# Performance work log

Hardware: AMD Instinct MI355X
Metric: run time of the kernel (lower is better)

## Reference

```python
import jax, jax.numpy as jnp
import numpy as np

B, D, E = 4096, 64, 1
NU, NI = 50000, 10000
H, HD = 4, 16          # MultiheadAttention(node_dim=64, num_heads=4)
GAMMA, LAM = 1.0, 0.5


def setup_inputs() -> dict:
    key = jax.random.key(0)
    ks = jax.random.split(key, 16)
    s = 0.05
    return {
        "u": jnp.arange(B, dtype=jnp.int32),                         # unique user ids
        "v": jax.random.randint(ks[0], (B,), 0, NI),
        "t": jax.random.normal(ks[1], (B,), jnp.float32),
        "delta_t": jax.random.uniform(ks[2], (B,), jnp.float32),
        "edge_feat": jax.random.normal(ks[3], (B, E), jnp.float32),
        "returns": jax.random.normal(ks[4], (NI,), jnp.float32),
        "cov_matrix": jax.random.normal(ks[5], (NI, NI), jnp.float32),
        "user_emb_w": jax.random.normal(ks[6], (NU, D), jnp.float32) * s,
        "item_emb_w": jax.random.normal(ks[7], (NI, D), jnp.float32) * s,
        "mem": jnp.zeros((NU, D), jnp.float32),                      # TGN memory (init zeros)
        "gru_w_ih": jax.random.normal(ks[8], (3 * D, 2 * D + 1 + E), jnp.float32) * s,
        "gru_w_hh": jax.random.normal(ks[9], (3 * D, D), jnp.float32) * s,
        "gru_b_ih": jnp.zeros((3 * D,), jnp.float32),
        "gru_b_hh": jnp.zeros((3 * D,), jnp.float32),
        "in_proj_w": jax.random.normal(ks[10], (3 * D, D), jnp.float32) * s,
        "in_proj_b": jnp.zeros((3 * D,), jnp.float32),
        "out_proj_w": jax.random.normal(ks[11], (D, D), jnp.float32) * s,
        "out_proj_b": jnp.zeros((D,), jnp.float32),
    }


def reference(u, v, t, delta_t, edge_feat, returns, cov_matrix,
              user_emb_w, item_emb_w, mem,
              gru_w_ih, gru_w_hh, gru_b_ih, gru_b_hh,
              in_proj_w, in_proj_b, out_proj_w, out_proj_b):
    u_emb = user_emb_w[u]                                  # [B, D]
    v_emb = item_emb_w[v]                                  # [B, D]

    # --- TGN memory update: gather -> GRUCell -> (scatter). u is unique per batch,
    # so the original per-node Python loop == one batched GRUCell step.
    msg = jnp.concatenate([u_emb, v_emb, delta_t[:, None], edge_feat], axis=1)  # [B, 2D+1+E]
    h = mem[u]                                             # [B, D]
    gi = msg @ gru_w_ih.T + gru_b_ih                       # [B, 3D]
    gh = h @ gru_w_hh.T + gru_b_hh                         # [B, 3D]
    i_r, i_z, i_n = jnp.split(gi, 3, axis=1)
    h_r, h_z, h_n = jnp.split(gh, 3, axis=1)
    r = jax.nn.sigmoid(i_r + h_r)
    z = jax.nn.sigmoid(i_z + h_z)
    n = jnp.tanh(i_n + r * h_n)
    h_new = (1.0 - z) * n + z * h                          # updated memory rows [B, D]

    # --- GraphAttention over a 2-token sequence [src, neighbor+edge]
    x = jnp.stack([u_emb, v_emb + edge_feat], axis=1)      # [B, 2, D] (edge_feat [B,1] broadcasts)
    qkv = x @ in_proj_w.T + in_proj_b                      # [B, 2, 3D]
    q, k, vv = jnp.split(qkv, 3, axis=-1)
    to_heads = lambda a: a.reshape(B, 2, H, HD).transpose(0, 2, 1, 3)  # [B, H, 2, HD]
    q, k, vv = to_heads(q), to_heads(k), to_heads(vv)
    attn = jax.nn.softmax(jnp.einsum("bhqd,bhkd->bhqk", q, k) * 0.25, axis=-1)  # 1/sqrt(16)
    o = jnp.einsum("bhqk,bhkd->bhqd", attn, vv).transpose(0, 2, 1, 3).reshape(B, 2, D)
    o = o @ out_proj_w.T + out_proj_b
    z_u = o[:, 0]                                          # [B, D]

    # --- portfolio scatter + MV scoring (portfolio starts empty; items added = v)
    cov_vals = cov_matrix[:, v].mean(axis=1)               # [NI] big irregular gather
    mv = returns / GAMMA - 0.5 * cov_vals                  # [NI]
    pref = jax.random.uniform(jax.random.key(42), (NI,), jnp.float32)
    combined = LAM * mv + (1.0 - LAM) * pref               # [NI]

    candidates = jnp.ones((B, NI), bool).at[jnp.arange(B), v].set(False)
    scores = jnp.where(candidates, combined[None, :], -jnp.inf)  # [B, NI]
    _, topk = jax.lax.top_k(scores, 4)
    pos_items = topk[:, 0]
    neg_items = topk[:, 1:4]
    return z_u, h_new, pos_items, neg_items
```

## Files before the change

### kernel.cpp

```cpp
#include <hip/hip_runtime.h>
#include <math.h>

#define BB_ 4096
#define DD_ 64
#define NI_ 10000

#define GRU_BLOCKS  256
#define ATT_BLOCKS  512
#define MV_BLOCKS   2500
#define BIG_BLOCKS  (GRU_BLOCKS + ATT_BLOCKS + MV_BLOCKS)

#define LDSF 13312

#define S1_BLOCKS 40

typedef unsigned long long u64;
typedef float v4f __attribute__((ext_vector_type(4)));

__device__ inline unsigned rotl32(unsigned x, unsigned r){ return (x<<r)|(x>>(32u-r)); }

__device__ inline float jax_uniform_key42(int i){
  const unsigned k0 = 0u, k1 = 42u;
  const unsigned ks2 = 0x1BD11BDAu ^ k0 ^ k1;
  unsigned x0 = 0u, x1 = (unsigned)i;
  unsigned ks[3] = {k0, k1, ks2};
  x0 += ks[0]; x1 += ks[1];
  const unsigned R0[4] = {13u,15u,26u,6u};
  const unsigned R1[4] = {17u,29u,16u,24u};
  #pragma unroll
  for (int it = 0; it < 5; ++it){
    const unsigned* R = (it & 1) ? R1 : R0;
    #pragma unroll
    for (int j = 0; j < 4; ++j){ x0 += x1; x1 = rotl32(x1, R[j]); x1 ^= x0; }
    x0 += ks[(it+1)%3];
    x1 += ks[(it+2)%3] + (unsigned)(it+1);
  }
  unsigned bits = x0 ^ x1;
  unsigned f = (bits >> 9) | 0x3F800000u;
  return __uint_as_float(f) - 1.0f;
}

__global__ __launch_bounds__(1024) void hist_kernel(
    const int* __restrict__ v, float* __restrict__ w_out)
{
  __shared__ float wl[NI_];
  const int tid = threadIdx.x;
  for (int i = tid; i < NI_; i += 1024) wl[i] = 0.0f;
  __syncthreads();
  for (int i = tid; i < BB_; i += 1024) atomicAdd(&wl[v[i]], 1.0f);
  __syncthreads();
  for (int i = tid; i < NI_; i += 1024) w_out[i] = wl[i];
}

__device__ inline float dot4v(v4f a, v4f b){
  return a.x*b.x + a.y*b.y + a.z*b.z + a.w*b.w;
}

__global__ __launch_bounds__(256, 3) void big_kernel(
    const int* __restrict__ u, const int* __restrict__ v,
    const float* __restrict__ delta_t, const float* __restrict__ edge_feat,
    const float* __restrict__ w_in, const float* __restrict__ returns,
    const float* __restrict__ cov, float* __restrict__ combined,
    const float* __restrict__ user_emb, const float* __restrict__ item_emb,
    const float* __restrict__ mem,
    const float* __restrict__ w_ih, const float* __restrict__ w_hh,
    const float* __restrict__ b_ih, const float* __restrict__ b_hh,
    const float* __restrict__ in_w, const float* __restrict__ in_b,
    const float* __restrict__ out_w, const float* __restrict__ out_b,
    float* __restrict__ h_new_out, float* __restrict__ z_out)
{
  __shared__ __align__(16) float S[LDSF];
  const int tid  = threadIdx.x;
  const int lane = tid & 63, wid = tid >> 6;
  const int bid  = blockIdx.x;

  if (bid >= GRU_BLOCKS + ATT_BLOCKS) {
    {
      const float4* src = (const float4*)w_in;
      float4* dst = (float4*)S;
      for (int i = tid; i < NI_/4; i += 256) dst[i] = src[i];
    }
    __syncthreads();

    const int row = (bid - (GRU_BLOCKS + ATT_BLOCKS)) * 4 + wid;
    const v4f* w4 = (const v4f*)S;
    const v4f* r4 = (const v4f*)(cov + (size_t)row * NI_);

    float a0 = 0.0f, a1 = 0.0f, a2 = 0.0f, a3 = 0.0f;
    int k = lane;
    #pragma unroll 1
    for (int it = 0; it < 9; ++it, k += 256) {
      v4f c0 = __builtin_nontemporal_load(&r4[k]);
      v4f c1 = __builtin_nontemporal_load(&r4[k+64]);
      v4f c2 = __builtin_nontemporal_load(&r4[k+128]);
      v4f c3 = __builtin_nontemporal_load(&r4[k+192]);
      v4f w0 = w4[k], w1 = w4[k+64], w2 = w4[k+128], w3 = w4[k+192];
      a0 += dot4v(c0, w0);
      a1 += dot4v(c1, w1);
      a2 += dot4v(c2, w2);
      a3 += dot4v(c3, w3);
    }
    #pragma unroll 1
    for (int it = 0; it < 3; ++it, k += 64) {
      v4f c0 = __builtin_nontemporal_load(&r4[k]);
      a0 += dot4v(c0, w4[k]);
    }
    if (lane < 4) {
      v4f c0 = __builtin_nontemporal_load(&r4[2496 + lane]);
      a1 += dot4v(c0, w4[2496 + lane]);
    }
    float acc = (a0 + a1) + (a2 + a3);
    #pragma unroll
    for (int off = 32; off > 0; off >>= 1) acc += __shfl_xor(acc, off);

    if (lane == 0) {
      float cov_val = acc * (1.0f / (float)BB_);
      float mv = returns[row] - 0.5f * cov_val;
      float pref = jax_uniform_key42(row);
      combined[row] = 0.5f * mv + 0.5f * pref;
    }
  } else if (bid < GRU_BLOCKS) {
    float* T  = S;
    float* BI = S + 12738;
    float* BH = S + 12930;
    const int rowbase = bid * 16 + wid * 4;

    if (tid < 192) { BI[tid] = b_ih[tid]; BH[tid] = b_hh[tid]; }

    float u_d[4], v_d[4], h_d[4], dt[4], ef[4];
    int bb[4];
    #pragma unroll
    for (int rr = 0; rr < 4; ++rr) {
      int b = rowbase + rr; bb[rr] = b;
      int uu = u[b], vv = v[b];
      u_d[rr] = user_emb[uu*64 + lane];
      v_d[rr] = item_emb[vv*64 + lane];
      h_d[rr] = mem[uu*64 + lane];
      dt[rr]  = delta_t[b];
      ef[rr]  = edge_feat[b];
    }

    for (int idx = tid; idx < 64*192; idx += 256) {
      int o = idx >> 6, j = idx & 63;
      T[j*193 + o] = w_ih[o*130 + j];
    }
    __syncthreads();

    float biR = BI[lane], biZ = BI[64+lane], biN = BI[128+lane];
    float bhR = BH[lane], bhZ = BH[64+lane], bhN = BH[128+lane];
    float accR[4], accZ[4], accN[4], hN[4];
    #pragma unroll
    for (int rr = 0; rr < 4; ++rr) { accR[rr]=biR+bhR; accZ[rr]=biZ+bhZ; accN[rr]=biN; hN[rr]=bhN; }

    for (int j = 0; j < 64; ++j) {
      float wR = T[j*193 + lane], wZ = T[j*193 + 64 + lane], wN = T[j*193 + 128 + lane];
      #pragma unroll
      for (int rr = 0; rr < 4; ++rr) {
        float m = __shfl(u_d[rr], j);
        accR[rr] = fmaf(wR, m, accR[rr]); accZ[rr] = fmaf(wZ, m, accZ[rr]); accN[rr] = fmaf(wN, m, accN[rr]);
      }
    }
    __syncthreads();

    for (int idx = tid; idx < 64*192; idx += 256) {
      int o = idx >> 6, j = idx & 63;
      T[j*193 + o] = w_ih[o*130 + 64 + j];
    }
    __syncthreads();
    for (int j = 0; j < 64; ++j) {
      float wR = T[j*193 + lane], wZ = T[j*193 + 64 + lane], wN = T[j*193 + 128 + lane];
      #pragma unroll
      for (int rr = 0; rr < 4; ++rr) {
        float m = __shfl(v_d[rr], j);
        accR[rr] = fmaf(wR, m, accR[rr]); accZ[rr] = fmaf(wZ, m, accZ[rr]); accN[rr] = fmaf(wN, m, accN[rr]);
      }
    }
    __syncthreads();

    for (int idx = tid; idx < 384; idx += 256) {
      int o = idx >> 1, c = idx & 1;
      T[c*193 + o] = w_ih[o*130 + 128 + c];
    }
    for (int idx = tid; idx < 64*192; idx += 256) {
      int o = idx >> 6, jj = idx & 63;
      T[(2+jj)*193 + o] = w_hh[idx];
    }
    __syncthreads();
    {
      float wR = T[lane], wZ = T[64 + lane], wN = T[128 + lane];
      float eR = T[193 + lane], eZ = T[193 + 64 + lane], eN = T[193 + 128 + lane];
      #pragma unroll
      for (int rr = 0; rr < 4; ++rr) {
        accR[rr] = fmaf(wR, dt[rr], accR[rr]); accZ[rr] = fmaf(wZ, dt[rr], accZ[rr]); accN[rr] = fmaf(wN, dt[rr], accN[rr]);
        accR[rr] = fmaf(eR, ef[rr], accR[rr]); accZ[rr] = fmaf(eZ, ef[rr], accZ[rr]); accN[rr] = fmaf(eN, ef[rr], accN[rr]);
      }
    }
    for (int jj = 0; jj < 64; ++jj) {
      int base = (2+jj)*193;
      float wR = T[base + lane], wZ = T[base + 64 + lane], wN = T[base + 128 + lane];
      #pragma unroll
      for (int rr = 0; rr < 4; ++rr) {
        float m = __shfl(h_d[rr], jj);
        accR[rr] = fmaf(wR, m, accR[rr]); accZ[rr] = fmaf(wZ, m, accZ[rr]); hN[rr] = fmaf(wN, m, hN[rr]);
      }
    }

    #pragma unroll
    for (int rr = 0; rr < 4; ++rr) {
      float r = 1.0f / (1.0f + expf(-accR[rr]));
      float z = 1.0f / (1.0f + expf(-accZ[rr]));
      float n = tanhf(accN[rr] + r * hN[rr]);
      float hn = (1.0f - z) * n + z * h_d[rr];
      h_new_out[bb[rr]*64 + lane] = hn;
    }
  } else {
    float* C    = S;
    float* OT   = S + 4160;
    float* BIN  = S + 8320;
    float* BOUT = S + 8512;
    const int abid = bid - GRU_BLOCKS;
    const int rowbase = abid * 8 + wid * 2;

    for (int idx = tid; idx < 64*64; idx += 256) {
      int k = idx >> 6, j = idx & 63;
      OT[j*65 + k] = out_w[idx];
    }
    if (tid < 192) BIN[tid] = in_b[tid];
    if (tid < 64)  BOUT[tid] = out_b[tid];

    float u_d[2], x1_d[2];
    int bb[2];
    #pragma unroll
    for (int rr = 0; rr < 2; ++rr) {
      int b = rowbase + rr; bb[rr] = b;
      int uu = u[b], vv = v[b];
      float ef = edge_feat[b];
      u_d[rr]  = user_emb[uu*64 + lane];
      x1_d[rr] = item_emb[vv*64 + lane] + ef;
    }

    float q0[2], k0[2], k1[2], v0[2], v1[2];

    for (int idx = tid; idx < 4096; idx += 256) {
      int o = idx >> 6, j = idx & 63;
      C[j*65 + o] = in_w[o*64 + j];
    }
    __syncthreads();
    {
      float bq = BIN[lane];
      #pragma unroll
      for (int rr = 0; rr < 2; ++rr) q0[rr] = bq;
      for (int j = 0; j < 64; ++j) {
        float wq = C[j*65 + lane];
        #pragma unroll
        for (int rr = 0; rr < 2; ++rr) q0[rr] = fmaf(wq, __shfl(u_d[rr], j), q0[rr]);
      }
    }
    __syncthreads();

    for (int idx = tid; idx < 4096; idx += 256) {
      int o = idx >> 6, j = idx & 63;
      C[j*65 + o] = in_w[(64+o)*64 + j];
    }
    __syncthreads();
    {
      float bk = BIN[64+lane];
      #pragma unroll
      for (int rr = 0; rr < 2; ++rr) { k0[rr] = bk; k1[rr] = bk; }
      for (int j = 0; j < 64; ++j) {
        float wk = C[j*65 + lane];
        #pragma unroll
        for (int rr = 0; rr < 2; ++rr) {
          k0[rr] = fmaf(wk, __shfl(u_d[rr], j),  k0[rr]);
          k1[rr] = fmaf(wk, __shfl(x1_d[rr], j), k1[rr]);
        }
      }
    }
    __syncthreads();

    for (int idx = tid; idx < 4096; idx += 256) {
      int o = idx >> 6, j = idx & 63;
      C[j*65 + o] = in_w[(128+o)*64 + j];
    }
    __syncthreads();
    {
      float bv = BIN[128+lane];
      #pragma unroll
      for (int rr = 0; rr < 2; ++rr) { v0[rr] = bv; v1[rr] = bv; }
      for (int j = 0; j < 64; ++j) {
        float wv = C[j*65 + lane];
        #pragma unroll
        for (int rr = 0; rr < 2; ++rr) {
          v0[rr] = fmaf(wv, __shfl(u_d[rr], j),  v0[rr]);
          v1[rr] = fmaf(wv, __shfl(x1_d[rr], j), v1[rr]);
        }
      }
    }

    #pragma unroll
    for (int rr = 0; rr < 2; ++rr) {
      float p0 = q0[rr]*k0[rr], p1 = q0[rr]*k1[rr];
      #pragma unroll
      for (int off = 1; off < 16; off <<= 1) { p0 += __shfl_xor(p0, off); p1 += __shfl_xor(p1, off); }
      float s0 = p0 * 0.25f, s1 = p1 * 0.25f;
      float m  = fmaxf(s0, s1);
      float e0 = expf(s0 - m), e1 = expf(s1 - m);
      float inv = 1.0f / (e0 + e1);
      float o_d = (e0 * v0[rr] + e1 * v1[rr]) * inv;
      float zacc = BOUT[lane];
      for (int j = 0; j < 64; ++j)
        zacc = fmaf(OT[j*65 + lane], __shfl(o_d, j), zacc);
      z_out[bb[rr]*64 + lane] = zacc;
    }
  }
}

__device__ inline u64 shfl_down_u64(u64 x, int off){
  unsigned lo = (unsigned)(x & 0xFFFFFFFFull), hi = (unsigned)(x >> 32);
  lo = __shfl_down(lo, off); hi = __shfl_down(hi, off);
  return ((u64)hi << 32) | (u64)lo;
}

__device__ inline u64 make_key(float val, int i){
  unsigned u = __float_as_uint(val);
  u ^= (u >> 31) ? 0xFFFFFFFFu : 0x80000000u;
  return ((u64)u << 32) | (u64)(0xFFFFFFFFu - (unsigned)i);
}

__global__ __launch_bounds__(256) void top5_stage1(
    const float* __restrict__ combined, u64* __restrict__ keys_out)
{
  __shared__ u64 redL[4];
  __shared__ u64 sel;
  const int tid = threadIdx.x, lane = tid & 63, wid = tid >> 6;
  const int i = blockIdx.x * 250 + tid;

  u64 key = 0ull;
  if (tid < 250 && i < NI_) key = make_key(combined[i], i);

  for (int r = 0; r < 5; ++r) {
    u64 best = key;
    #pragma unroll
    for (int off = 32; off > 0; off >>= 1) {
      u64 o = shfl_down_u64(best, off);
      if (o > best) best = o;
    }
    if (lane == 0) redL[wid] = best;
    __syncthreads();
    if (tid == 0) {
      u64 b = redL[0];
      for (int wv = 1; wv < 4; ++wv) if (redL[wv] > b) b = redL[wv];
      sel = b;
      keys_out[blockIdx.x * 5 + r] = b;
    }
    __syncthreads();
    if (key == sel) key = 0ull;
  }
}

__global__ __launch_bounds__(256) void top5_stage2(
    const u64* __restrict__ keys_in, const int* __restrict__ v,
    float* __restrict__ pos_out, float* __restrict__ neg_out)
{
  __shared__ u64 redL[4];
  __shared__ u64 sel;
  __shared__ int chosen[5];
  const int tid = threadIdx.x, lane = tid & 63, wid = tid >> 6;

  u64 key = (tid < 5 * S1_BLOCKS) ? keys_in[tid] : 0ull;

  for (int r = 0; r < 5; ++r) {
    u64 best = key;
    #pragma unroll
    for (int off = 32; off > 0; off >>= 1) {
      u64 o = shfl_down_u64(best, off);
      if (o > best) best = o;
    }
    if (lane == 0) redL[wid] = best;
    __syncthreads();
    if (tid == 0) {
      u64 b = redL[0];
      for (int wv = 1; wv < 4; ++wv) if (redL[wv] > b) b = redL[wv];
      sel = b;
      chosen[r] = (int)(0xFFFFFFFFu - (unsigned)(b & 0xFFFFFFFFull));
    }
    __syncthreads();
    if (key == sel) key = 0ull;
  }

  const int b = blockIdx.x * 256 + tid;
  int vb = v[b];
  int f[4]; int n = 0;
  #pragma unroll
  for (int c = 0; c < 5; ++c) { if (n < 4 && chosen[c] != vb) f[n++] = chosen[c]; }
  pos_out[b]       = (float)f[0];
  neg_out[b*3 + 0] = (float)f[1];
  neg_out[b*3 + 1] = (float)f[2];
  neg_out[b*3 + 2] = (float)f[3];
}

extern "C" void kernel_launch(void* const* d_in, const int* in_sizes, int n_in,
                              void* d_out, int out_size, void* d_ws, size_t ws_size,
                              hipStream_t stream)
{
  const int*   u        = (const int*)d_in[0];
  const int*   v        = (const int*)d_in[1];
  const float* delta_t  = (const float*)d_in[3];
  const float* edge_f   = (const float*)d_in[4];
  const float* returns  = (const float*)d_in[5];
  const float* cov      = (const float*)d_in[6];
  const float* user_emb = (const float*)d_in[7];
  const float* item_emb = (const float*)d_in[8];
  const float* mem      = (const float*)d_in[9];
  const float* w_ih     = (const float*)d_in[10];
  const float* w_hh     = (const float*)d_in[11];
  const float* b_ih     = (const float*)d_in[12];
  const float* b_hh     = (const float*)d_in[13];
  const float* in_w     = (const float*)d_in[14];
  const float* in_b     = (const float*)d_in[15];
  const float* out_w    = (const float*)d_in[16];
  const float* out_b    = (const float*)d_in[17];

  float* out     = (float*)d_out;
  float* z_out   = out;
  float* h_out   = out + BB_*DD_;
  float* pos_out = out + 2*BB_*DD_;
  float* neg_out = out + 2*BB_*DD_ + BB_;

  float* ws        = (float*)d_ws;
  float* w_hist    = ws;
  float* combined  = ws + 10240;
  u64*   keys      = (u64*)(ws + 20480);

  hipLaunchKernelGGL(hist_kernel, dim3(1), dim3(1024), 0, stream, v, w_hist);
  hipLaunchKernelGGL(big_kernel, dim3(BIG_BLOCKS), dim3(256), 0, stream,
                     u, v, delta_t, edge_f, w_hist, returns, cov, combined,
                     user_emb, item_emb, mem, w_ih, w_hh, b_ih, b_hh,
                     in_w, in_b, out_w, out_b, h_out, z_out);
  hipLaunchKernelGGL(top5_stage1, dim3(S1_BLOCKS), dim3(256), 0, stream,
                     combined, keys);
  hipLaunchKernelGGL(top5_stage2, dim3(16), dim3(256), 0, stream,
                     keys, v, pos_out, neg_out);
}
```

Measured before the change: 116.5 us.

## Shrink big_kernel LDS footprint to double occupancy

Cuts the shared-memory buffer roughly in half and raises the launch-bounds occupancy hint from 3 to 6 blocks per CU. The MV blocks now read the weight vector straight from global memory instead of staging it in LDS. The GRU blocks stream the combined weight columns through a 32-column LDS tile. The attention blocks reuse one LDS buffer for the output projection after the QKV pass. The intent is more concurrent waves to hide latency on the bandwidth-bound covariance stream, at the cost of extra barriers, extra global/L2 reads of the weights, and possible register pressure from the tighter bound.

```diff
diff --git a/kernel.cpp b/kernel.cpp
--- a/kernel.cpp
+++ b/kernel.cpp
@@ -10,7 +10,7 @@
 #define MV_BLOCKS   2500
 #define BIG_BLOCKS  (GRU_BLOCKS + ATT_BLOCKS + MV_BLOCKS)
 
-#define LDSF 13312
+#define LDSF 6560
 
 #define S1_BLOCKS 40
 
@@ -56,7 +56,7 @@
   return a.x*b.x + a.y*b.y + a.z*b.z + a.w*b.w;
 }
 
-__global__ __launch_bounds__(256, 3) void big_kernel(
+__global__ __launch_bounds__(256, 6) void big_kernel(
     const int* __restrict__ u, const int* __restrict__ v,
     const float* __restrict__ delta_t, const float* __restrict__ edge_feat,
     const float* __restrict__ w_in, const float* __restrict__ returns,
@@ -75,15 +75,8 @@
   const int bid  = blockIdx.x;
 
   if (bid >= GRU_BLOCKS + ATT_BLOCKS) {
-    {
-      const float4* src = (const float4*)w_in;
-      float4* dst = (float4*)S;
-      for (int i = tid; i < NI_/4; i += 256) dst[i] = src[i];
-    }
-    __syncthreads();
-
     const int row = (bid - (GRU_BLOCKS + ATT_BLOCKS)) * 4 + wid;
-    const v4f* w4 = (const v4f*)S;
+    const v4f* w4 = (const v4f*)w_in;
     const v4f* r4 = (const v4f*)(cov + (size_t)row * NI_);
 
     float a0 = 0.0f, a1 = 0.0f, a2 = 0.0f, a3 = 0.0f;
@@ -121,8 +114,8 @@
     }
   } else if (bid < GRU_BLOCKS) {
     float* T  = S;
-    float* BI = S + 12738;
-    float* BH = S + 12930;
+    float* BI = S + 6176;
+    float* BH = S + 6368;
     const int rowbase = bid * 16 + wid * 4;
 
     if (tid < 192) { BI[tid] = b_ih[tid]; BH[tid] = b_hh[tid]; }
@@ -140,68 +133,45 @@
       ef[rr]  = edge_feat[b];
     }
 
-    for (int idx = tid; idx < 64*192; idx += 256) {
-      int o = idx >> 6, j = idx & 63;
-      T[j*193 + o] = w_ih[o*130 + j];
-    }
-    __syncthreads();
-
-    float biR = BI[lane], biZ = BI[64+lane], biN = BI[128+lane];
-    float bhR = BH[lane], bhZ = BH[64+lane], bhN = BH[128+lane];
     float accR[4], accZ[4], accN[4], hN[4];
-    #pragma unroll
-    for (int rr = 0; rr < 4; ++rr) { accR[rr]=biR+bhR; accZ[rr]=biZ+bhZ; accN[rr]=biN; hN[rr]=bhN; }
-
-    for (int j = 0; j < 64; ++j) {
-      float wR = T[j*193 + lane], wZ = T[j*193 + 64 + lane], wN = T[j*193 + 128 + lane];
-      #pragma unroll
-      for (int rr = 0; rr < 4; ++rr) {
-        float m = __shfl(u_d[rr], j);
-        accR[rr] = fmaf(wR, m, accR[rr]); accZ[rr] = fmaf(wZ, m, accZ[rr]); accN[rr] = fmaf(wN, m, accN[rr]);
-      }
-    }
-    __syncthreads();
-
-    for (int idx = tid; idx < 64*192; idx += 256) {
-      int o = idx >> 6, j = idx & 63;
-      T[j*193 + o] = w_ih[o*130 + 64 + j];
-    }
-    __syncthreads();
-    for (int j = 0; j < 64; ++j) {
-      float wR = T[j*193 + lane], wZ = T[j*193 + 64 + lane], wN = T[j*193 + 128 + lane];
-      #pragma unroll
-      for (int rr = 0; rr < 4; ++rr) {
-        float m = __shfl(v_d[rr], j);
-        accR[rr] = fmaf(wR, m, accR[rr]); accZ[rr] = fmaf(wZ, m, accZ[rr]); accN[rr] = fmaf(wN, m, accN[rr]);
-      }
-    }
-    __syncthreads();
-
-    for (int idx = tid; idx < 384; idx += 256) {
-      int o = idx >> 1, c = idx & 1;
-      T[c*193 + o] = w_ih[o*130 + 128 + c];
-    }
-    for (int idx = tid; idx < 64*192; idx += 256) {
-      int o = idx >> 6, jj = idx & 63;
-      T[(2+jj)*193 + o] = w_hh[idx];
-    }
-    __syncthreads();
-    {
-      float wR = T[lane], wZ = T[64 + lane], wN = T[128 + lane];
-      float eR = T[193 + lane], eZ = T[193 + 64 + lane], eN = T[193 + 128 + lane];
-      #pragma unroll
-      for (int rr = 0; rr < 4; ++rr) {
-        accR[rr] = fmaf(wR, dt[rr], accR[rr]); accZ[rr] = fmaf(wZ, dt[rr], accZ[rr]); accN[rr] = fmaf(wN, dt[rr], accN[rr]);
-        accR[rr] = fmaf(eR, ef[rr], accR[rr]); accZ[rr] = fmaf(eZ, ef[rr], accZ[rr]); accN[rr] = fmaf(eN, ef[rr], accN[rr]);
-      }
-    }
-    for (int jj = 0; jj < 64; ++jj) {
-      int base = (2+jj)*193;
-      float wR = T[base + lane], wZ = T[base + 64 + lane], wN = T[base + 128 + lane];
-      #pragma unroll
-      for (int rr = 0; rr < 4; ++rr) {
-        float m = __shfl(h_d[rr], jj);
-        accR[rr] = fmaf(wR, m, accR[rr]); accZ[rr] = fmaf(wZ, m, accZ[rr]); hN[rr] = fmaf(wN, m, hN[rr]);
+    bool init = false;
+
+    for (int c = 0; c < 194; c += 32) {
+      const int ncols = (194 - c < 32) ? (194 - c) : 32;
+      __syncthreads();
+      for (int idx = tid; idx < ncols*192; idx += 256) {
+        int cc = idx / 192, o = idx - cc*192;
+        int col = c + cc;
+        T[cc*193 + o] = (col < 130) ? w_ih[o*130 + col] : w_hh[o*64 + (col-130)];
+      }
+      __syncthreads();
+
+      if (!init) {
+        init = true;
+        float biR = BI[lane], biZ = BI[64+lane], biN = BI[128+lane];
+        float bhR = BH[lane], bhZ = BH[64+lane], bhN = BH[128+lane];
+        #pragma unroll
+        for (int rr = 0; rr < 4; ++rr) { accR[rr]=biR+bhR; accZ[rr]=biZ+bhZ; accN[rr]=biN; hN[rr]=bhN; }
+      }
+
+      for (int cc = 0; cc < ncols; ++cc) {
+        const int col = c + cc;
+        float wR = T[cc*193 + lane], wZ = T[cc*193 + 64 + lane], wN = T[cc*193 + 128 + lane];
+        if (col < 130) {
+          #pragma unroll
+          for (int rr = 0; rr < 4; ++rr) {
+            float m = (col < 64)  ? __shfl(u_d[rr], col)
+                    : (col < 128) ? __shfl(v_d[rr], col-64)
+                    : (col == 128) ? dt[rr] : ef[rr];
+            accR[rr] = fmaf(wR, m, accR[rr]); accZ[rr] = fmaf(wZ, m, accZ[rr]); accN[rr] = fmaf(wN, m, accN[rr]);
+          }
+        } else {
+          #pragma unroll
+          for (int rr = 0; rr < 4; ++rr) {
+            float m = __shfl(h_d[rr], col-130);
+            accR[rr] = fmaf(wR, m, accR[rr]); accZ[rr] = fmaf(wZ, m, accZ[rr]); hN[rr] = fmaf(wN, m, hN[rr]);
+          }
+        }
       }
     }
 
@@ -215,16 +185,11 @@
     }
   } else {
     float* C    = S;
-    float* OT   = S + 4160;
-    float* BIN  = S + 8320;
-    float* BOUT = S + 8512;
+    float* BIN  = S + 4160;
+    float* BOUT = S + 4352;
     const int abid = bid - GRU_BLOCKS;
     const int rowbase = abid * 8 + wid * 2;
 
-    for (int idx = tid; idx < 64*64; idx += 256) {
-      int k = idx >> 6, j = idx & 63;
-      OT[j*65 + k] = out_w[idx];
-    }
     if (tid < 192) BIN[tid] = in_b[tid];
     if (tid < 64)  BOUT[tid] = out_b[tid];
 
@@ -296,6 +261,13 @@
         }
       }
     }
+    __syncthreads();
+
+    for (int idx = tid; idx < 4096; idx += 256) {
+      int k = idx >> 6, j = idx & 63;
+      C[j*65 + k] = out_w[idx];
+    }
+    __syncthreads();
 
     #pragma unroll
     for (int rr = 0; rr < 2; ++rr) {
@@ -309,7 +281,7 @@
       float o_d = (e0 * v0[rr] + e1 * v1[rr]) * inv;
       float zacc = BOUT[lane];
       for (int j = 0; j < 64; ++j)
-        zacc = fmaf(OT[j*65 + lane], __shfl(o_d, j), zacc);
+        zacc = fmaf(C[j*65 + lane], __shfl(o_d, j), zacc);
       z_out[bb[rr]*64 + lane] = zacc;
     }
   }
```

Measured after the change: 150.1 us. 28.8% more time.
